# Kernel tuning notes

Measured on AMD Instinct MI355X. Metric: run time of the kernel, lower is better.

The kernel has to match this reference:

```python
import jax, jax.numpy as jnp
import numpy as np

N = 50000      # nodes
E = 800000     # edges (before self-loops)
IN = 256       # in_channels
H = 4          # heads (layer 1)
C = 64         # hidden per head
OUT = 40       # out_channels / classes


def setup_inputs() -> dict:
    key = jax.random.key(0)
    ks = jax.random.split(key, 10)
    s = 0.05  # weight init scale
    return {
        "x": jax.random.normal(ks[0], (N, IN), jnp.float32),
        "edge_index": jax.random.randint(ks[1], (2, E), 0, N),
        "W1": jax.random.normal(ks[2], (IN, H * C), jnp.float32) * s,
        "a_src1": jax.random.normal(ks[3], (H, C), jnp.float32) * s,
        "a_dst1": jax.random.normal(ks[4], (H, C), jnp.float32) * s,
        "b1": jnp.zeros((H * C,), jnp.float32),
        "W2": jax.random.normal(ks[5], (H * C, OUT), jnp.float32) * s,
        "a_src2": jax.random.normal(ks[6], (1, OUT), jnp.float32) * s,
        "a_dst2": jax.random.normal(ks[7], (1, OUT), jnp.float32) * s,
        "b2": jnp.zeros((OUT,), jnp.float32),
    }


def _gat_layer(x, src, dst, W, a_src, a_dst, bias, heads, out_c):
    """PyG GATConv (concat=True, negative_slope=0.2, self-loops already in src/dst)."""
    n = x.shape[0]
    h = (x @ W).reshape(n, heads, out_c)                    # [N,H,C]
    al_s = jnp.sum(h * a_src, axis=-1)                      # [N,H]
    al_d = jnp.sum(h * a_dst, axis=-1)                      # [N,H]
    e = jax.nn.leaky_relu(al_s[src] + al_d[dst], 0.2)       # [Etot,H]
    # edge softmax over incoming edges of each destination node
    m = jax.ops.segment_max(e, dst, num_segments=n)         # [N,H]
    ee = jnp.exp(e - m[dst])
    denom = jax.ops.segment_sum(ee, dst, num_segments=n)
    alpha = ee / (denom[dst] + 1e-16)                       # [Etot,H]
    msg = alpha[:, :, None] * h[src]                        # [Etot,H,C]
    out = jax.ops.segment_sum(msg, dst, num_segments=n)     # [N,H,C]
    return out.reshape(n, heads * out_c) + bias


def reference(x, edge_index, W1, a_src1, a_dst1, b1, W2, a_src2, a_dst2, b2):
    n = x.shape[0]
    loops = jnp.arange(n, dtype=edge_index.dtype)
    src = jnp.concatenate([edge_index[0], loops])
    dst = jnp.concatenate([edge_index[1], loops])
    h = _gat_layer(x, src, dst, W1, a_src1, a_dst1, b1, H, C)   # [N, H*C]
    h = jax.nn.relu(h)
    # F.dropout in eval mode is identity (reference run in eval mode)
    out = _gat_layer(h, src, dst, W2, a_src2, a_dst2, b2, 1, OUT)  # [N, OUT]
    return jax.nn.log_softmax(out, axis=1)
```

## Files before the change

### kernel.cpp

```cpp
#include <hip/hip_runtime.h>
#include <hip/hip_bf16.h>

typedef __hip_bfloat16 bf16;
typedef short v8s __attribute__((ext_vector_type(8)));
typedef float v4f __attribute__((ext_vector_type(4)));
typedef float v2f __attribute__((ext_vector_type(2)));

constexpr int NN    = 50000;
constexpr int NE    = 800000;
constexpr int CIN   = 256;
constexpr int HC    = 256;
constexpr int NH    = 4;
constexpr int NOUT  = 40;
constexpr int NPAD  = 48;
constexpr int SCB   = 196;
constexpr int B1    = 128;
constexpr int CH    = (NE + B1 - 1) / B1;
constexpr int NB    = (NN + 255) >> 8;

constexpr size_t al256(size_t x){ return (x + 255) & ~(size_t)255; }
constexpr size_t WS_FLAGS = 0;
constexpr size_t WS_EW1   = 256;
constexpr size_t WS_W1T   = al256(WS_EW1   + (size_t)NE*16);
constexpr size_t WS_AS1N  = al256(WS_W1T   + (size_t)CIN*HC*2);
constexpr size_t WS_AD1N  = al256(WS_AS1N  + HC*2);
constexpr size_t WS_B1N   = al256(WS_AD1N  + HC*2);
constexpr size_t WS_W2T   = al256(WS_B1N   + HC*2);
constexpr size_t WS_AS2N  = al256(WS_W2T   + (size_t)NPAD*HC*2);
constexpr size_t WS_AD2N  = al256(WS_AS2N  + NOUT*2);
constexpr size_t WS_B2N   = al256(WS_AD2N  + NOUT*2);
constexpr size_t WS_COUNTS= al256(WS_B2N   + NOUT*2);
constexpr size_t WS_CURSOR= al256(WS_COUNTS+ (size_t)NN*4);
constexpr size_t WS_ROWPTR= al256(WS_CURSOR+ (size_t)NN*4);
constexpr size_t WS_EIDX  = al256(WS_ROWPTR+ (size_t)(NN+1)*4);
constexpr size_t WS_H1    = al256(WS_EIDX  + (size_t)NE*4);
constexpr size_t WS_ALS1  = al256(WS_H1    + (size_t)NN*HC);
constexpr size_t WS_ALD1  = al256(WS_ALS1  + (size_t)NN*NH*4);
constexpr size_t WS_Y1    = al256(WS_ALD1  + (size_t)NN*NH*4);
constexpr size_t WS_H2    = al256(WS_Y1    + (size_t)NN*HC*2);
constexpr size_t WS_ALS2  = al256(WS_H2    + (size_t)NN*64);
constexpr size_t WS_ALD2  = al256(WS_ALS2  + (size_t)NN*4);
constexpr size_t WS_EW2   = al256(WS_ALD2  + (size_t)NN*4);
constexpr size_t WS_BSUM  = al256(WS_EW2   + (size_t)NE*4);
constexpr size_t WS_BOFF  = al256(WS_BSUM  + 1024);
constexpr size_t WS_GCNT  = al256(WS_BOFF  + 1024);
constexpr size_t WS_ROFF  = al256(WS_GCNT  + (size_t)256*B1*4);
constexpr size_t WS_BBASE = al256(WS_ROFF  + (size_t)256*B1*4);
constexpr size_t WS_EBUF  = al256(WS_BBASE + 1056);

constexpr int CV_W1  = 0;
constexpr int CV_AS1 = CV_W1  + CIN*HC;
constexpr int CV_AD1 = CV_AS1 + HC;
constexpr int CV_B1  = CV_AD1 + HC;
constexpr int CV_W2  = CV_B1  + HC;
constexpr int CV_AS2 = CV_W2  + HC*NOUT;
constexpr int CV_AD2 = CV_AS2 + NOUT;
constexpr int CV_B2  = CV_AD2 + NOUT;
constexpr int CV_HIST= CV_B2  + NOUT;
constexpr int CV_END = CV_HIST + NE;

__device__ __forceinline__ float b2f(bf16 v) { return __bfloat162float(v); }
__device__ __forceinline__ bf16  f2b(float v){ return __float2bfloat16(v); }
__device__ __forceinline__ float bits2f(unsigned short u){ return __uint_as_float(((unsigned)u) << 16); }
__device__ __forceinline__ unsigned short f2bits(float v){
  bf16 t = __float2bfloat16(v);
  return *reinterpret_cast<unsigned short*>(&t);
}
__device__ __forceinline__ float lrelu(float x){ return x > 0.f ? x : 0.2f * x; }

__device__ __forceinline__ float wave_sum(float v){
  #pragma unroll
  for (int off = 32; off; off >>= 1) v += __shfl_xor(v, off, 64);
  return v;
}
__device__ __forceinline__ float wave_max(float v){
  #pragma unroll
  for (int off = 32; off; off >>= 1) v = fmaxf(v, __shfl_xor(v, off, 64));
  return v;
}

__global__ __launch_bounds__(64) void k_detect(const unsigned short* __restrict__ xu,
                                               const unsigned* __restrict__ eu,
                                               int* __restrict__ flags){
  int lane = threadIdx.x;
  int cnt = 0;
  for (int i = lane; i < 256; i += 64){
    int e = (xu[i] >> 7) & 0xFF;
    cnt += (e >= 0x60 && e <= 0x8F) ? 1 : 0;
  }
  #pragma unroll
  for (int off = 32; off; off >>= 1) cnt += __shfl_xor(cnt, off, 64);
  unsigned odd = eu[2 * lane + 1];
  #pragma unroll
  for (int off = 32; off; off >>= 1) odd |= __shfl_xor(odd, off, 64);
  if (lane == 0){
    flags[0] = (cnt < 218) ? 1 : 0;
    flags[1] = (odd == 0)  ? 1 : 0;
  }
}

__device__ __forceinline__ bf16 cvt_b(const void* src, int i, int f32m){
  if (f32m) return __float2bfloat16(((const float*)src)[i]);
  return ((const bf16*)src)[i];
}

__global__ __launch_bounds__(256) void k_convert(
    const void* __restrict__ W1,
    const void* __restrict__ as1,const void* __restrict__ ad1,
    const void* __restrict__ b1, const void* __restrict__ W2,
    const void* __restrict__ as2,const void* __restrict__ ad2,
    const void* __restrict__ b2, const void* __restrict__ ei,
    char* __restrict__ ws){
  const int* flags = (const int*)(ws + WS_FLAGS);
  int f32m = flags[0], i64m = flags[1];
  bf16* w1t  = (bf16*)(ws + WS_W1T);
  bf16* as1n = (bf16*)(ws + WS_AS1N);
  bf16* ad1n = (bf16*)(ws + WS_AD1N);
  bf16* b1n  = (bf16*)(ws + WS_B1N);
  bf16* w2t  = (bf16*)(ws + WS_W2T);
  bf16* as2n = (bf16*)(ws + WS_AS2N);
  bf16* ad2n = (bf16*)(ws + WS_AD2N);
  bf16* b2n  = (bf16*)(ws + WS_B2N);
  int*  counts=(int*) (ws + WS_COUNTS);
  for (int g = blockIdx.x * 256 + threadIdx.x; g < CV_END; g += gridDim.x * 256){
    if      (g < CV_AS1){ int i = g-CV_W1; int k = i >> 8, n = i & 255;
      w1t[n*CIN + k] = cvt_b(W1, i, f32m); }
    else if (g < CV_AD1) as1n[g-CV_AS1] = cvt_b(as1,g-CV_AS1, f32m);
    else if (g < CV_B1 ) ad1n[g-CV_AD1] = cvt_b(ad1,g-CV_AD1, f32m);
    else if (g < CV_W2 ) b1n [g-CV_B1 ] = cvt_b(b1, g-CV_B1,  f32m);
    else if (g < CV_AS2){ int i = g-CV_W2; int k = i / NOUT, n = i - k*NOUT;
      w2t[n*CIN + k] = cvt_b(W2, i, f32m); }
    else if (g < CV_AD2) as2n[g-CV_AS2] = cvt_b(as2,g-CV_AS2, f32m);
    else if (g < CV_B2 ) ad2n[g-CV_AD2] = cvt_b(ad2,g-CV_AD2, f32m);
    else if (g < CV_HIST) b2n[g-CV_B2 ] = cvt_b(b2, g-CV_B2,  f32m);
    else { int i = g-CV_HIST;
      int d = i64m ? (int)((const long long*)ei)[(size_t)NE+i] : ((const int*)ei)[NE+i];
      atomicAdd(&counts[d], 1); }
  }
}

__global__ __launch_bounds__(256) void k_scan_part(const int* __restrict__ counts, int* __restrict__ bsum){
  __shared__ int lds[256];
  int t = threadIdx.x;
  int idx = blockIdx.x * 256 + t;
  int v = (idx < NN) ? counts[idx] : 0;
  lds[t] = v;
  #pragma unroll
  for (int s = 128; s > 0; s >>= 1){
    __syncthreads();
    if (t < s) lds[t] += lds[t + s];
  }
  if (t == 0) bsum[blockIdx.x] = lds[0];
}

__global__ __launch_bounds__(256) void k_scan_mid(const int* __restrict__ bsum, int* __restrict__ boff,
                                                  int* __restrict__ row_ptr){
  __shared__ int lds[256];
  int t = threadIdx.x;
  int v = (t < SCB) ? bsum[t] : 0;
  lds[t] = v;
  for (int off = 1; off < 256; off <<= 1){
    __syncthreads();
    int u = (t >= off) ? lds[t - off] : 0;
    __syncthreads();
    lds[t] += u;
  }
  __syncthreads();
  if (t < SCB) boff[t] = lds[t] - v;
  if (t == 0) row_ptr[NN] = NE;
}

__global__ __launch_bounds__(256) void k_scan_apply(const int* __restrict__ counts, const int* __restrict__ boff,
                                                    int* __restrict__ row_ptr){
  __shared__ int lds[256];
  int t = threadIdx.x;
  int idx = blockIdx.x * 256 + t;
  int v = (idx < NN) ? counts[idx] : 0;
  lds[t] = v;
  for (int off = 1; off < 256; off <<= 1){
    __syncthreads();
    int u = (t >= off) ? lds[t - off] : 0;
    __syncthreads();
    lds[t] += u;
  }
  __syncthreads();
  if (idx < NN) row_ptr[idx] = boff[blockIdx.x] + lds[t] - v;
}

__global__ __launch_bounds__(256) void k_lhist(const void* __restrict__ ei, const int* __restrict__ flags,
                                               int* __restrict__ gcnt){
  __shared__ int h[256];
  int tid = threadIdx.x, blk = blockIdx.x;
  h[tid] = 0;
  __syncthreads();
  int i0 = blk * CH, i1 = min(i0 + CH, NE);
  int i64m = flags[1];
  for (int i = i0 + tid; i < i1; i += 256){
    int d = i64m ? (int)((const long long*)ei)[(size_t)NE + i] : ((const int*)ei)[NE + i];
    atomicAdd(&h[d >> 8], 1);
  }
  __syncthreads();
  gcnt[tid * B1 + blk] = h[tid];
}

__global__ __launch_bounds__(256) void k_gscan(const int* __restrict__ gcnt, int* __restrict__ roff,
                                               int* __restrict__ bbase){
  __shared__ int lds[256];
  int t = threadIdx.x;
  int tot = 0;
  for (int blk = 0; blk < B1; ++blk) tot += gcnt[t * B1 + blk];
  lds[t] = tot;
  for (int off = 1; off < 256; off <<= 1){
    __syncthreads();
    int u = (t >= off) ? lds[t - off] : 0;
    __syncthreads();
    lds[t] += u;
  }
  __syncthreads();
  int base = lds[t] - tot;
  bbase[t] = base;
  if (t == 255) bbase[256] = NE;
  int run = base;
  for (int blk = 0; blk < B1; ++blk){
    roff[t * B1 + blk] = run;
    run += gcnt[t * B1 + blk];
  }
}

__global__ __launch_bounds__(256) void k_bscatter(const void* __restrict__ ei, const int* __restrict__ flags,
                                                  const int* __restrict__ roff, int2* __restrict__ ebuf){
  __shared__ int lcur[256];
  int tid = threadIdx.x, blk = blockIdx.x;
  lcur[tid] = roff[tid * B1 + blk];
  __syncthreads();
  int i0 = blk * CH, i1 = min(i0 + CH, NE);
  int i64m = flags[1];
  for (int i = i0 + tid; i < i1; i += 256){
    int s, d;
    if (i64m){ s = (int)((const long long*)ei)[i]; d = (int)((const long long*)ei)[(size_t)NE + i]; }
    else     { s = ((const int*)ei)[i];            d = ((const int*)ei)[NE + i]; }
    int pos = atomicAdd(&lcur[d >> 8], 1);
    ebuf[pos] = make_int2(s, d);
  }
}

__global__ __launch_bounds__(256) void k_refine(const int2* __restrict__ ebuf, const int* __restrict__ bbase,
                                                const int* __restrict__ row_ptr, int* __restrict__ cursor,
                                                int* __restrict__ eidx){
  int b = blockIdx.x;
  int p0 = bbase[b], p1 = bbase[b + 1];
  for (int p = p0 + threadIdx.x; p < p1; p += 256){
    int2 e = ebuf[p];
    int pos = row_ptr[e.y] + atomicAdd(&cursor[e.y], 1);
    eidx[pos] = e.x;
  }
}

constexpr int G1R = 128;
__global__ __launch_bounds__(256, 2) void k_gemm1(const void* __restrict__ xin,
                                               const int* __restrict__ flags,
                                               const bf16* __restrict__ w1t,
                                               const bf16* __restrict__ as1, const bf16* __restrict__ ad1,
                                               unsigned char* __restrict__ h1q,
                                               float* __restrict__ al_s1, float* __restrict__ al_d1){
  __shared__ __align__(16) short Ab[G1R * 64];
  __shared__ __align__(16) short Bb[256 * 64];
  int tid  = threadIdx.x;
  int w    = tid >> 6, lane = tid & 63, quad = lane >> 4, c = lane & 15;
  int row0 = blockIdx.x * G1R;
  int f32m = flags[0];

  v4f acc[2][4][4];
  #pragma unroll
  for (int mh = 0; mh < 2; ++mh)
    #pragma unroll
    for (int mt = 0; mt < 4; ++mt)
      #pragma unroll
      for (int nt = 0; nt < 4; ++nt) acc[mh][mt][nt] = (v4f){0.f,0.f,0.f,0.f};

  int arow = tid >> 2, aseg = tid & 3;
  int asw  = arow & 7;
  int grow0 = row0 + arow;      if (grow0 >= NN) grow0 = NN - 1;
  int grow1 = row0 + 64 + arow; if (grow1 >= NN) grow1 = NN - 1;
  int bsw  = tid & 7;

  float4 afl[2][4];
  v8s    abf[2][2];
  v8s    breg[8];

  auto loadA = [&](int ph){
    if (f32m){
      const float* s0 = (const float*)xin + (size_t)grow0 * CIN + ph*64 + aseg*16;
      const float* s1 = (const float*)xin + (size_t)grow1 * CIN + ph*64 + aseg*16;
      #pragma unroll
      for (int i = 0; i < 4; ++i){ afl[0][i] = *reinterpret_cast<const float4*>(s0 + i*4);
                                   afl[1][i] = *reinterpret_cast<const float4*>(s1 + i*4); }
    } else {
      const short* s0 = (const short*)xin + (size_t)grow0 * CIN + ph*64 + aseg*16;
      const short* s1 = (const short*)xin + (size_t)grow1 * CIN + ph*64 + aseg*16;
      abf[0][0] = *reinterpret_cast<const v8s*>(s0);
      abf[0][1] = *reinterpret_cast<const v8s*>(s0 + 8);
      abf[1][0] = *reinterpret_cast<const v8s*>(s1);
      abf[1][1] = *reinterpret_cast<const v8s*>(s1 + 8);
    }
  };
  auto loadB = [&](int ph){
    const short* src = (const short*)w1t + (size_t)tid * CIN + ph*64;
    #pragma unroll
    for (int j = 0; j < 8; ++j) breg[j] = *reinterpret_cast<const v8s*>(src + j*8);
  };
  auto stageA = [&](){
    #pragma unroll
    for (int mh = 0; mh < 2; ++mh){
      short* dst = &Ab[(mh*64 + arow) * 64];
      if (f32m){
        #pragma unroll
        for (int k = 0; k < 2; ++k){
          v8s t;
          t[0] = (short)f2bits(afl[mh][2*k].x);   t[1] = (short)f2bits(afl[mh][2*k].y);
          t[2] = (short)f2bits(afl[mh][2*k].z);   t[3] = (short)f2bits(afl[mh][2*k].w);
          t[4] = (short)f2bits(afl[mh][2*k+1].x); t[5] = (short)f2bits(afl[mh][2*k+1].y);
          t[6] = (short)f2bits(afl[mh][2*k+1].z); t[7] = (short)f2bits(afl[mh][2*k+1].w);
          *reinterpret_cast<v8s*>(dst + (((aseg*2 + k) ^ asw) << 3)) = t;
        }
      } else {
        #pragma unroll
        for (int k = 0; k < 2; ++k)
          *reinterpret_cast<v8s*>(dst + (((aseg*2 + k) ^ asw) << 3)) = abf[mh][k];
      }
    }
  };
  auto stageB = [&](){
    short* dst = &Bb[tid * 64];
    #pragma unroll
    for (int j = 0; j < 8; ++j)
      *reinterpret_cast<v8s*>(dst + ((j ^ bsw) << 3)) = breg[j];
  };

  loadA(0); loadB(0);
  #pragma unroll
  for (int ph = 0; ph < 4; ++ph){
    if (ph) __syncthreads();
    stageA(); stageB();
    __syncthreads();
    if (ph < 3){ loadA(ph + 1); loadB(ph + 1); }
    #pragma unroll
    for (int s = 0; s < 2; ++s){
      int ch = s*4 + quad;
      int sl = (ch ^ (c & 7)) << 3;
      v8s bfb[4];
      #pragma unroll
      for (int nt = 0; nt < 4; ++nt)
        bfb[nt] = *reinterpret_cast<const v8s*>(&Bb[(w*64 + nt*16 + c) * 64 + sl]);
      #pragma unroll
      for (int mh = 0; mh < 2; ++mh){
        v8s af[4];
        #pragma unroll
        for (int mt = 0; mt < 4; ++mt)
          af[mt] = *reinterpret_cast<const v8s*>(&Ab[(mh*64 + mt*16 + c) * 64 + sl]);
        #pragma unroll
        for (int mt = 0; mt < 4; ++mt)
          #pragma unroll
          for (int nt = 0; nt < 4; ++nt)
            acc[mh][mt][nt] = __builtin_amdgcn_mfma_f32_16x16x32_bf16(af[mt], bfb[nt], acc[mh][mt][nt], 0, 0, 0);
      }
    }
  }

  float as1v[4], ad1v[4];
  #pragma unroll
  for (int nt = 0; nt < 4; ++nt){
    as1v[nt] = b2f(as1[w*64 + nt*16 + c]);
    ad1v[nt] = b2f(ad1[w*64 + nt*16 + c]);
  }
  #pragma unroll
  for (int mh = 0; mh < 2; ++mh){
    int rowb = row0 + mh*64;
    #pragma unroll
    for (int mt = 0; mt < 4; ++mt){
      #pragma unroll
      for (int r = 0; r < 4; ++r){
        float ps = 0.f, pd = 0.f;
        #pragma unroll
        for (int nt = 0; nt < 4; ++nt){ ps += acc[mh][mt][nt][r] * as1v[nt]; pd += acc[mh][mt][nt][r] * ad1v[nt]; }
        #pragma unroll
        for (int off = 1; off < 16; off <<= 1){ ps += __shfl_xor(ps, off, 64); pd += __shfl_xor(pd, off, 64); }
        int row = rowb + mt*16 + quad*4 + r;
        if (c == 0 && row < NN){
          al_s1[row * NH + w] = ps;
          al_d1[row * NH + w] = pd;
        }
      }
    }
    #pragma unroll
    for (int mt = 0; mt < 4; ++mt){
      #pragma unroll
      for (int nt = 0; nt < 4; ++nt){
        #pragma unroll
        for (int r = 0; r < 4; r += 2){
          int row = rowb + mt*16 + quad*4 + r;
          if (row + 1 < NN){
            int pk = __builtin_amdgcn_cvt_pk_fp8_f32(acc[mh][mt][nt][r], acc[mh][mt][nt][r+1], 0, false);
            size_t col = w*64 + nt*16 + c;
            h1q[(size_t)row       * HC + col] = (unsigned char)(pk & 0xFF);
            h1q[(size_t)(row + 1) * HC + col] = (unsigned char)((pk >> 8) & 0xFF);
          } else if (row < NN){
            int pk = __builtin_amdgcn_cvt_pk_fp8_f32(acc[mh][mt][nt][r], acc[mh][mt][nt][r], 0, false);
            h1q[(size_t)row * HC + w*64 + nt*16 + c] = (unsigned char)(pk & 0xFF);
          }
        }
      }
    }
  }
}

#define ACCPK(W, U) { \
  v2f _lo = __builtin_amdgcn_cvt_pk_f32_fp8((int)(U), false); \
  v2f _hi = __builtin_amdgcn_cvt_pk_f32_fp8((int)(U), true);  \
  a0 += (W) * _lo.x; a1 += (W) * _lo.y;                       \
  a2 += (W) * _hi.x; a3 += (W) * _hi.y; }

__global__ __launch_bounds__(256) void k_gather1(const int* __restrict__ row_ptr, const int* __restrict__ eidx,
                                                 const float* __restrict__ al_s1, const float* __restrict__ al_d1,
                                                 const unsigned* __restrict__ h1v, const bf16* __restrict__ b1,
                                                 bf16* __restrict__ y1){
  int lane = threadIdx.x & 63;
  int n = blockIdx.x * 4 + (threadIdx.x >> 6);
  int h = lane >> 4;
  int p0 = __builtin_amdgcn_readfirstlane(row_ptr[n]);
  int p1 = __builtin_amdgcn_readfirstlane(row_ptr[n + 1]);
  float ad_h = al_d1[n * NH + h];
  float wss = __expf(lrelu(al_s1[n * NH + h] + ad_h));
  unsigned us = h1v[(size_t)n * 64 + lane];
  float den = wss;
  float a0 = 0.f, a1 = 0.f, a2 = 0.f, a3 = 0.f;
  ACCPK(wss, us)
  int p = p0;
  for (; p + 3 < p1; p += 4){
    int sA = __builtin_amdgcn_readfirstlane(eidx[p]);
    int sB = __builtin_amdgcn_readfirstlane(eidx[p + 1]);
    int sC = __builtin_amdgcn_readfirstlane(eidx[p + 2]);
    int sD = __builtin_amdgcn_readfirstlane(eidx[p + 3]);
    float wA = __expf(lrelu(al_s1[sA * NH + h] + ad_h));
    float wB = __expf(lrelu(al_s1[sB * NH + h] + ad_h));
    float wC = __expf(lrelu(al_s1[sC * NH + h] + ad_h));
    float wD = __expf(lrelu(al_s1[sD * NH + h] + ad_h));
    unsigned uA = h1v[(size_t)sA * 64 + lane];
    unsigned uB = h1v[(size_t)sB * 64 + lane];
    unsigned uC = h1v[(size_t)sC * 64 + lane];
    unsigned uD = h1v[(size_t)sD * 64 + lane];
    den += (wA + wB) + (wC + wD);
    ACCPK(wA, uA)
    ACCPK(wB, uB)
    ACCPK(wC, uC)
    ACCPK(wD, uD)
  }
  for (; p < p1; ++p){
    int s = __builtin_amdgcn_readfirstlane(eidx[p]);
    float w = __expf(lrelu(al_s1[s * NH + h] + ad_h));
    unsigned u = h1v[(size_t)s * 64 + lane];
    den += w;
    ACCPK(w, u)
  }
  float inv = 1.f / (den + 1e-16f);
  ushort4 bb = reinterpret_cast<const ushort4*>(b1)[lane];
  ushort4 o;
  o.x = f2bits(fmaxf(a0 * inv + bits2f(bb.x), 0.f));
  o.y = f2bits(fmaxf(a1 * inv + bits2f(bb.y), 0.f));
  o.z = f2bits(fmaxf(a2 * inv + bits2f(bb.z), 0.f));
  o.w = f2bits(fmaxf(a3 * inv + bits2f(bb.w), 0.f));
  reinterpret_cast<ushort4*>(y1)[(size_t)n * 64 + lane] = o;
}

constexpr int W2LP = 260;
__global__ __launch_bounds__(256) void k_gemm2(const bf16* __restrict__ y1, const bf16* __restrict__ w2t,
                                               const bf16* __restrict__ as2, const bf16* __restrict__ ad2,
                                               unsigned char* __restrict__ h2q, float* __restrict__ al_s2,
                                               float* __restrict__ al_d2){
  __shared__ short Wb[NPAD * W2LP];
  int tid = threadIdx.x;
  int w = tid >> 6, lane = tid & 63, quad = lane >> 4, c = lane & 15;
  int m0 = blockIdx.x * 64 + w * 16;
  for (int idx = tid; idx < NPAD * 32; idx += 256){
    int n = idx >> 5, sg = idx & 31;
    *reinterpret_cast<v8s*>(&Wb[n * W2LP + sg * 8]) =
      *reinterpret_cast<const v8s*>((const short*)w2t + (size_t)n * CIN + sg * 8);
  }
  int arow = m0 + c; if (arow >= NN) arow = NN - 1;
  const short* ar = (const short*)y1 + (size_t)arow * HC + quad * 8;
  v8s a[8];
  #pragma unroll
  for (int i = 0; i < 8; ++i) a[i] = *reinterpret_cast<const v8s*>(ar + i * 32);
  __syncthreads();

  v4f acc[3];
  #pragma unroll
  for (int t = 0; t < 3; ++t) acc[t] = (v4f){0.f, 0.f, 0.f, 0.f};
  #pragma unroll
  for (int k = 0; k < 8; ++k){
    int ch = k*4 + quad;
    #pragma unroll
    for (int t = 0; t < 3; ++t){
      v8s b = *reinterpret_cast<const v8s*>(&Wb[(t*16 + c) * W2LP + ch * 8]);
      acc[t] = __builtin_amdgcn_mfma_f32_16x16x32_bf16(a[k], b, acc[t], 0, 0, 0);
    }
  }
  float as2f[3], ad2f[3];
  #pragma unroll
  for (int t = 0; t < 3; ++t){
    int col = t*16 + c;
    as2f[t] = (col < NOUT) ? b2f(as2[col]) : 0.f;
    ad2f[t] = (col < NOUT) ? b2f(ad2[col]) : 0.f;
  }
  #pragma unroll
  for (int r = 0; r < 4; ++r){
    int row = m0 + quad*4 + r;
    float ps = 0.f, pd = 0.f;
    #pragma unroll
    for (int t = 0; t < 3; ++t){ ps += acc[t][r] * as2f[t]; pd += acc[t][r] * ad2f[t]; }
    #pragma unroll
    for (int off = 1; off < 16; off <<= 1){ ps += __shfl_xor(ps, off, 64); pd += __shfl_xor(pd, off, 64); }
    if (row < NN && c == 0){ al_s2[row] = ps; al_d2[row] = pd; }
  }
  #pragma unroll
  for (int t = 0; t < 3; ++t){
    int col = t*16 + c;
    if (col < NOUT){
      #pragma unroll
      for (int r = 0; r < 4; r += 2){
        int row = m0 + quad*4 + r;
        int pk = __builtin_amdgcn_cvt_pk_fp8_f32(acc[t][r], acc[t][r+1], 0, false);
        if (row < NN)     h2q[(size_t)row       * 64 + col] = (unsigned char)(pk & 0xFF);
        if (row + 1 < NN) h2q[(size_t)(row + 1) * 64 + col] = (unsigned char)((pk >> 8) & 0xFF);
      }
    }
  }
}

__global__ __launch_bounds__(256) void k_gather2(const int* __restrict__ row_ptr, const int* __restrict__ eidx,
                                                 const float* __restrict__ al_s2, const float* __restrict__ al_d2,
                                                 const unsigned char* __restrict__ h2q, const bf16* __restrict__ b2v,
                                                 const int* __restrict__ flags, void* __restrict__ out){
  int lane = threadIdx.x & 63;
  int n = blockIdx.x * 4 + (threadIdx.x >> 6);
  int q = lane >> 4, c = lane & 15;
  bool act = (c < 10);
  int p0 = __builtin_amdgcn_readfirstlane(row_ptr[n]);
  int p1 = __builtin_amdgcn_readfirstlane(row_ptr[n + 1]);
  const unsigned* h2v = reinterpret_cast<const unsigned*>(h2q);
  float adn = al_d2[n];
  float den = 0.f, a0 = 0.f, a1 = 0.f, a2 = 0.f, a3 = 0.f;
  if (q == 0){
    float wss = __expf(lrelu(al_s2[n] + adn));
    den = wss;
    if (act){
      unsigned u = h2v[(size_t)n * 16 + c];
      ACCPK(wss, u)
    }
  }
  int p = p0 + q;
  for (; p + 4 < p1; p += 8){
    int sA = eidx[p], sB = eidx[p + 4];
    float wA = __expf(lrelu(al_s2[sA] + adn));
    float wB = __expf(lrelu(al_s2[sB] + adn));
    unsigned uA = act ? h2v[(size_t)sA * 16 + c] : 0u;
    unsigned uB = act ? h2v[(size_t)sB * 16 + c] : 0u;
    den += wA + wB;
    ACCPK(wA, uA)
    ACCPK(wB, uB)
  }
  if (p < p1){
    int s = eidx[p];
    float w = __expf(lrelu(al_s2[s] + adn));
    unsigned u = act ? h2v[(size_t)s * 16 + c] : 0u;
    den += w;
    ACCPK(w, u)
  }
  #pragma unroll
  for (int off = 16; off <= 32; off <<= 1){
    den += __shfl_xor(den, off, 64);
    a0  += __shfl_xor(a0,  off, 64);
    a1  += __shfl_xor(a1,  off, 64);
    a2  += __shfl_xor(a2,  off, 64);
    a3  += __shfl_xor(a3,  off, 64);
  }
  float inv = 1.f / (den + 1e-16f);
  float v0 = -INFINITY, v1 = -INFINITY, v2 = -INFINITY, v3 = -INFINITY;
  if (act){
    ushort4 bb = *reinterpret_cast<const ushort4*>(reinterpret_cast<const unsigned short*>(b2v) + 4 * c);
    v0 = a0 * inv + bits2f(bb.x);
    v1 = a1 * inv + bits2f(bb.y);
    v2 = a2 * inv + bits2f(bb.z);
    v3 = a3 * inv + bits2f(bb.w);
  }
  float M = wave_max(fmaxf(fmaxf(v0, v1), fmaxf(v2, v3)));
  float ex = (q == 0 && act)
           ? (__expf(v0 - M) + __expf(v1 - M)) + (__expf(v2 - M) + __expf(v3 - M)) : 0.f;
  float S = wave_sum(ex);
  if (q == 0 && act){
    float lg = M + __logf(S);
    if (flags[0]){
      float4 o = {v0 - lg, v1 - lg, v2 - lg, v3 - lg};
      *reinterpret_cast<float4*>((float*)out + (size_t)n * NOUT + 4 * c) = o;
    } else {
      ushort4 o;
      o.x = f2bits(v0 - lg); o.y = f2bits(v1 - lg);
      o.z = f2bits(v2 - lg); o.w = f2bits(v3 - lg);
      *reinterpret_cast<ushort4*>((unsigned short*)out + (size_t)n * NOUT + 4 * c) = o;
    }
  }
}

extern "C" void kernel_launch(void* const* d_in, const int* in_sizes, int n_in,
                              void* d_out, int out_size, void* d_ws, size_t ws_size,
                              hipStream_t stream) {
  const void* x   = d_in[0];
  const void* ei  = d_in[1];
  const void* W1  = d_in[2];
  const void* as1 = d_in[3];
  const void* ad1 = d_in[4];
  const void* b1  = d_in[5];
  const void* W2  = d_in[6];
  const void* as2 = d_in[7];
  const void* ad2 = d_in[8];
  const void* b2  = d_in[9];

  char* ws = (char*)d_ws;
  int*   flags   = (int*)  (ws + WS_FLAGS);
  bf16*  w1t     = (bf16*) (ws + WS_W1T);
  bf16*  as1n    = (bf16*) (ws + WS_AS1N);
  bf16*  ad1n    = (bf16*) (ws + WS_AD1N);
  bf16*  b1n     = (bf16*) (ws + WS_B1N);
  bf16*  w2t     = (bf16*) (ws + WS_W2T);
  bf16*  as2n    = (bf16*) (ws + WS_AS2N);
  bf16*  ad2n    = (bf16*) (ws + WS_AD2N);
  bf16*  b2n     = (bf16*) (ws + WS_B2N);
  int*   counts  = (int*)  (ws + WS_COUNTS);
  int*   cursor  = (int*)  (ws + WS_CURSOR);
  int*   row_ptr = (int*)  (ws + WS_ROWPTR);
  int*   eidx    = (int*)  (ws + WS_EIDX);
  unsigned char* h1q = (unsigned char*)(ws + WS_H1);
  float* al_s1   = (float*)(ws + WS_ALS1);
  float* al_d1   = (float*)(ws + WS_ALD1);
  bf16*  y1      = (bf16*) (ws + WS_Y1);
  unsigned char* h2q = (unsigned char*)(ws + WS_H2);
  float* al_s2   = (float*)(ws + WS_ALS2);
  float* al_d2   = (float*)(ws + WS_ALD2);
  int*   bsum    = (int*)  (ws + WS_BSUM);
  int*   boff    = (int*)  (ws + WS_BOFF);
  int*   gcnt    = (int*)  (ws + WS_GCNT);
  int*   roff    = (int*)  (ws + WS_ROFF);
  int*   bbase   = (int*)  (ws + WS_BBASE);
  int2*  ebuf    = (int2*) (ws + WS_EBUF);

  hipMemsetAsync(counts, 0, (size_t)NN * 4, stream);
  hipMemsetAsync(cursor, 0, (size_t)NN * 4, stream);
  hipMemsetAsync(w2t,    0, (size_t)NPAD * CIN * 2, stream);

  k_detect <<<1, 64, 0, stream>>>((const unsigned short*)x, (const unsigned*)ei, flags);
  k_convert<<<1024, 256, 0, stream>>>(W1, as1, ad1, b1, W2, as2, ad2, b2, ei, ws);

  k_lhist   <<<B1, 256, 0, stream>>>(ei, flags, gcnt);
  k_gscan   <<<1, 256, 0, stream>>>(gcnt, roff, bbase);
  k_scan_part <<<SCB, 256, 0, stream>>>(counts, bsum);
  k_scan_mid  <<<1, 256, 0, stream>>>(bsum, boff, row_ptr);
  k_scan_apply<<<SCB, 256, 0, stream>>>(counts, boff, row_ptr);
  k_bscatter<<<B1, 256, 0, stream>>>(ei, flags, roff, ebuf);
  k_refine  <<<NB, 256, 0, stream>>>(ebuf, bbase, row_ptr, cursor, eidx);

  k_gemm1  <<<(NN + G1R - 1) / G1R, 256, 0, stream>>>(x, flags, w1t, as1n, ad1n, h1q, al_s1, al_d1);
  k_gather1<<<NN / 4, 256, 0, stream>>>(row_ptr, eidx, al_s1, al_d1, (const unsigned*)h1q, b1n, y1);
  k_gemm2  <<<(NN + 63) / 64, 256, 0, stream>>>(y1, w2t, as2n, ad2n, h2q, al_s2, al_d2);
  k_gather2<<<NN / 4, 256, 0, stream>>>(row_ptr, eidx, al_s2, al_d2, h2q, b2n, flags, d_out);
}
```

Measured before the change: 308.7 us.

## Fuse preprocessing launches: merge memsets/detect, histograms, and scans; unroll gather2

Three memsets and the format-detect kernel are replaced by one init kernel. The per-node degree count and the bucket histogram now run together in dedicated blocks of the convert kernel, which removes a separate pass over the edge list. The two small scan kernels run as two blocks of one launch. These changes are meant to cut launch overhead and one read of the destination indices. The layer-2 gather also gets a 4-way unrolled edge loop for more memory-level parallelism, at the cost of more registers.

```diff
diff --git a/kernel.cpp b/kernel.cpp
--- a/kernel.cpp
+++ b/kernel.cpp
@@ -56,8 +56,7 @@
 constexpr int CV_AS2 = CV_W2  + HC*NOUT;
 constexpr int CV_AD2 = CV_AS2 + NOUT;
 constexpr int CV_B2  = CV_AD2 + NOUT;
-constexpr int CV_HIST= CV_B2  + NOUT;
-constexpr int CV_END = CV_HIST + NE;
+constexpr int CV_END = CV_B2  + NOUT;
 
 __device__ __forceinline__ float b2f(bf16 v) { return __bfloat162float(v); }
 __device__ __forceinline__ bf16  f2b(float v){ return __float2bfloat16(v); }
@@ -79,23 +78,41 @@
   return v;
 }
 
-__global__ __launch_bounds__(64) void k_detect(const unsigned short* __restrict__ xu,
-                                               const unsigned* __restrict__ eu,
-                                               int* __restrict__ flags){
-  int lane = threadIdx.x;
-  int cnt = 0;
-  for (int i = lane; i < 256; i += 64){
-    int e = (xu[i] >> 7) & 0xFF;
-    cnt += (e >= 0x60 && e <= 0x8F) ? 1 : 0;
-  }
-  #pragma unroll
-  for (int off = 32; off; off >>= 1) cnt += __shfl_xor(cnt, off, 64);
-  unsigned odd = eu[2 * lane + 1];
-  #pragma unroll
-  for (int off = 32; off; off >>= 1) odd |= __shfl_xor(odd, off, 64);
-  if (lane == 0){
-    flags[0] = (cnt < 218) ? 1 : 0;
-    flags[1] = (odd == 0)  ? 1 : 0;
+constexpr int INIT_B = (2*NN + 2048 + 255) / 256;
+__global__ __launch_bounds__(256) void k_init(const unsigned short* __restrict__ xu,
+                                              const unsigned* __restrict__ eu,
+                                              char* __restrict__ ws){
+  int b = blockIdx.x;
+  if (b == INIT_B){
+    int lane = threadIdx.x;
+    if (lane < 64){
+      int* flags = (int*)(ws + WS_FLAGS);
+      int cnt = 0;
+      for (int i = lane; i < 256; i += 64){
+        int e = (xu[i] >> 7) & 0xFF;
+        cnt += (e >= 0x60 && e <= 0x8F) ? 1 : 0;
+      }
+      #pragma unroll
+      for (int off = 32; off; off >>= 1) cnt += __shfl_xor(cnt, off, 64);
+      unsigned odd = eu[2 * lane + 1];
+      #pragma unroll
+      for (int off = 32; off; off >>= 1) odd |= __shfl_xor(odd, off, 64);
+      if (lane == 0){
+        flags[0] = (cnt < 218) ? 1 : 0;
+        flags[1] = (odd == 0)  ? 1 : 0;
+      }
+    }
+    return;
+  }
+  int g = b * 256 + threadIdx.x;
+  int* counts = (int*)(ws + WS_COUNTS);
+  int* cursor = (int*)(ws + WS_CURSOR);
+  bf16* w2t   = (bf16*)(ws + WS_W2T);
+  if (g < NN) counts[g] = 0;
+  else if (g < 2*NN) cursor[g - NN] = 0;
+  else if (g < 2*NN + 2048){
+    int i = g - 2*NN;
+    w2t[(NOUT + (i >> 8)) * CIN + (i & 255)] = f2b(0.f);
   }
 }
 
@@ -113,6 +130,23 @@
     char* __restrict__ ws){
   const int* flags = (const int*)(ws + WS_FLAGS);
   int f32m = flags[0], i64m = flags[1];
+  int blk = blockIdx.x, tid = threadIdx.x;
+  if (blk < B1){
+    __shared__ int h[256];
+    int* counts = (int*)(ws + WS_COUNTS);
+    int* gcnt   = (int*)(ws + WS_GCNT);
+    h[tid] = 0;
+    __syncthreads();
+    int i0 = blk * CH, i1 = min(i0 + CH, NE);
+    for (int i = i0 + tid; i < i1; i += 256){
+      int d = i64m ? (int)((const long long*)ei)[(size_t)NE + i] : ((const int*)ei)[NE + i];
+      atomicAdd(&counts[d], 1);
+      atomicAdd(&h[d >> 8], 1);
+    }
+    __syncthreads();
+    gcnt[tid * B1 + blk] = h[tid];
+    return;
+  }
   bf16* w1t  = (bf16*)(ws + WS_W1T);
   bf16* as1n = (bf16*)(ws + WS_AS1N);
   bf16* ad1n = (bf16*)(ws + WS_AD1N);
@@ -121,8 +155,7 @@
   bf16* as2n = (bf16*)(ws + WS_AS2N);
   bf16* ad2n = (bf16*)(ws + WS_AD2N);
   bf16* b2n  = (bf16*)(ws + WS_B2N);
-  int*  counts=(int*) (ws + WS_COUNTS);
-  for (int g = blockIdx.x * 256 + threadIdx.x; g < CV_END; g += gridDim.x * 256){
+  for (int g = (blk - B1) * 256 + tid; g < CV_END; g += (gridDim.x - B1) * 256){
     if      (g < CV_AS1){ int i = g-CV_W1; int k = i >> 8, n = i & 255;
       w1t[n*CIN + k] = cvt_b(W1, i, f32m); }
     else if (g < CV_AD1) as1n[g-CV_AS1] = cvt_b(as1,g-CV_AS1, f32m);
@@ -132,10 +165,7 @@
       w2t[n*CIN + k] = cvt_b(W2, i, f32m); }
     else if (g < CV_AD2) as2n[g-CV_AS2] = cvt_b(as2,g-CV_AS2, f32m);
     else if (g < CV_B2 ) ad2n[g-CV_AD2] = cvt_b(ad2,g-CV_AD2, f32m);
-    else if (g < CV_HIST) b2n[g-CV_B2 ] = cvt_b(b2, g-CV_B2,  f32m);
-    else { int i = g-CV_HIST;
-      int d = i64m ? (int)((const long long*)ei)[(size_t)NE+i] : ((const int*)ei)[NE+i];
-      atomicAdd(&counts[d], 1); }
+    else                 b2n [g-CV_B2 ] = cvt_b(b2, g-CV_B2,  f32m);
   }
 }
 
@@ -153,21 +183,44 @@
   if (t == 0) bsum[blockIdx.x] = lds[0];
 }
 
-__global__ __launch_bounds__(256) void k_scan_mid(const int* __restrict__ bsum, int* __restrict__ boff,
-                                                  int* __restrict__ row_ptr){
+__global__ __launch_bounds__(256) void k_scan_mid2(const int* __restrict__ bsum, int* __restrict__ boff,
+                                                   int* __restrict__ row_ptr,
+                                                   const int* __restrict__ gcnt, int* __restrict__ roff,
+                                                   int* __restrict__ bbase){
   __shared__ int lds[256];
   int t = threadIdx.x;
-  int v = (t < SCB) ? bsum[t] : 0;
-  lds[t] = v;
-  for (int off = 1; off < 256; off <<= 1){
-    __syncthreads();
-    int u = (t >= off) ? lds[t - off] : 0;
-    __syncthreads();
-    lds[t] += u;
-  }
-  __syncthreads();
-  if (t < SCB) boff[t] = lds[t] - v;
-  if (t == 0) row_ptr[NN] = NE;
+  if (blockIdx.x == 0){
+    int v = (t < SCB) ? bsum[t] : 0;
+    lds[t] = v;
+    for (int off = 1; off < 256; off <<= 1){
+      __syncthreads();
+      int u = (t >= off) ? lds[t - off] : 0;
+      __syncthreads();
+      lds[t] += u;
+    }
+    __syncthreads();
+    if (t < SCB) boff[t] = lds[t] - v;
+    if (t == 0) row_ptr[NN] = NE;
+  } else {
+    int tot = 0;
+    for (int blk = 0; blk < B1; ++blk) tot += gcnt[t * B1 + blk];
+    lds[t] = tot;
+    for (int off = 1; off < 256; off <<= 1){
+      __syncthreads();
+      int u = (t >= off) ? lds[t - off] : 0;
+      __syncthreads();
+      lds[t] += u;
+    }
+    __syncthreads();
+    int base = lds[t] - tot;
+    bbase[t] = base;
+    if (t == 255) bbase[256] = NE;
+    int run = base;
+    for (int blk = 0; blk < B1; ++blk){
+      roff[t * B1 + blk] = run;
+      run += gcnt[t * B1 + blk];
+    }
+  }
 }
 
 __global__ __launch_bounds__(256) void k_scan_apply(const int* __restrict__ counts, const int* __restrict__ boff,
@@ -185,46 +238,6 @@
   }
   __syncthreads();
   if (idx < NN) row_ptr[idx] = boff[blockIdx.x] + lds[t] - v;
-}
-
-__global__ __launch_bounds__(256) void k_lhist(const void* __restrict__ ei, const int* __restrict__ flags,
-                                               int* __restrict__ gcnt){
-  __shared__ int h[256];
-  int tid = threadIdx.x, blk = blockIdx.x;
-  h[tid] = 0;
-  __syncthreads();
-  int i0 = blk * CH, i1 = min(i0 + CH, NE);
-  int i64m = flags[1];
-  for (int i = i0 + tid; i < i1; i += 256){
-    int d = i64m ? (int)((const long long*)ei)[(size_t)NE + i] : ((const int*)ei)[NE + i];
-    atomicAdd(&h[d >> 8], 1);
-  }
-  __syncthreads();
-  gcnt[tid * B1 + blk] = h[tid];
-}
-
-__global__ __launch_bounds__(256) void k_gscan(const int* __restrict__ gcnt, int* __restrict__ roff,
-                                               int* __restrict__ bbase){
-  __shared__ int lds[256];
-  int t = threadIdx.x;
-  int tot = 0;
-  for (int blk = 0; blk < B1; ++blk) tot += gcnt[t * B1 + blk];
-  lds[t] = tot;
-  for (int off = 1; off < 256; off <<= 1){
-    __syncthreads();
-    int u = (t >= off) ? lds[t - off] : 0;
-    __syncthreads();
-    lds[t] += u;
-  }
-  __syncthreads();
-  int base = lds[t] - tot;
-  bbase[t] = base;
-  if (t == 255) bbase[256] = NE;
-  int run = base;
-  for (int blk = 0; blk < B1; ++blk){
-    roff[t * B1 + blk] = run;
-    run += gcnt[t * B1 + blk];
-  }
 }
 
 __global__ __launch_bounds__(256) void k_bscatter(const void* __restrict__ ei, const int* __restrict__ flags,
@@ -559,6 +572,22 @@
     }
   }
   int p = p0 + q;
+  for (; p + 12 < p1; p += 16){
+    int sA = eidx[p], sB = eidx[p + 4], sC = eidx[p + 8], sD = eidx[p + 12];
+    float wA = __expf(lrelu(al_s2[sA] + adn));
+    float wB = __expf(lrelu(al_s2[sB] + adn));
+    float wC = __expf(lrelu(al_s2[sC] + adn));
+    float wD = __expf(lrelu(al_s2[sD] + adn));
+    unsigned uA = act ? h2v[(size_t)sA * 16 + c] : 0u;
+    unsigned uB = act ? h2v[(size_t)sB * 16 + c] : 0u;
+    unsigned uC = act ? h2v[(size_t)sC * 16 + c] : 0u;
+    unsigned uD = act ? h2v[(size_t)sD * 16 + c] : 0u;
+    den += (wA + wB) + (wC + wD);
+    ACCPK(wA, uA)
+    ACCPK(wB, uB)
+    ACCPK(wC, uC)
+    ACCPK(wD, uD)
+  }
   for (; p + 4 < p1; p += 8){
     int sA = eidx[p], sB = eidx[p + 4];
     float wA = __expf(lrelu(al_s2[sA] + adn));
@@ -653,17 +682,11 @@
   int*   bbase   = (int*)  (ws + WS_BBASE);
   int2*  ebuf    = (int2*) (ws + WS_EBUF);
 
-  hipMemsetAsync(counts, 0, (size_t)NN * 4, stream);
-  hipMemsetAsync(cursor, 0, (size_t)NN * 4, stream);
-  hipMemsetAsync(w2t,    0, (size_t)NPAD * CIN * 2, stream);
-
-  k_detect <<<1, 64, 0, stream>>>((const unsigned short*)x, (const unsigned*)ei, flags);
-  k_convert<<<1024, 256, 0, stream>>>(W1, as1, ad1, b1, W2, as2, ad2, b2, ei, ws);
-
-  k_lhist   <<<B1, 256, 0, stream>>>(ei, flags, gcnt);
-  k_gscan   <<<1, 256, 0, stream>>>(gcnt, roff, bbase);
+  k_init    <<<INIT_B + 1, 256, 0, stream>>>((const unsigned short*)x, (const unsigned*)ei, ws);
+  k_convert <<<1024, 256, 0, stream>>>(W1, as1, ad1, b1, W2, as2, ad2, b2, ei, ws);
+
   k_scan_part <<<SCB, 256, 0, stream>>>(counts, bsum);
-  k_scan_mid  <<<1, 256, 0, stream>>>(bsum, boff, row_ptr);
+  k_scan_mid2 <<<2, 256, 0, stream>>>(bsum, boff, row_ptr, gcnt, roff, bbase);
   k_scan_apply<<<SCB, 256, 0, stream>>>(counts, boff, row_ptr);
   k_bscatter<<<B1, 256, 0, stream>>>(ei, flags, roff, ebuf);
   k_refine  <<<NB, 256, 0, stream>>>(ebuf, bbase, row_ptr, cursor, eidx);
```

After: 290.4 us. 5.9% less time.
